# Performance work log

Hardware: AMD Instinct MI355X
Metric: run time of the kernel (lower is better)

The kernel has to match this reference:

```python
import jax, jax.numpy as jnp
import numpy as np


def _cdist_p2(x, y):
    # x: [B, N, D], y: [B, M, D] -> [B, N, M] euclidean distances
    x2 = jnp.sum(x * x, axis=-1, keepdims=True)          # [B, N, 1]
    y2 = jnp.sum(y * y, axis=-1, keepdims=True)          # [B, M, 1]
    xy = jnp.einsum('bnd,bmd->bnm', x, y)                # [B, N, M]
    d2 = x2 + jnp.swapaxes(y2, -1, -2) - 2.0 * xy
    return jnp.sqrt(jnp.maximum(d2, 0.0))


def setup_inputs() -> dict:
    key = jax.random.key(0)
    kx, ky = jax.random.split(key)
    B, N, M, D = 8, 8192, 8192, 64
    x = jax.random.normal(kx, (B, N, D), dtype=jnp.float32)
    y = jax.random.normal(ky, (B, M, D), dtype=jnp.float32)
    return {"x": x, "y": y}


def reference(x, y):
    # relative_distances: [B, N, M]
    rd = _cdist_p2(x, y)
    M = rd.shape[-1]
    a = jnp.min(rd, axis=-1)            # [B, N] nearest y for each x
    b = jnp.min(rd, axis=-2)            # [B, M] nearest x for each y
    loss_per_batch = jnp.sum(a, axis=-1) + jnp.sum(b, axis=-1)  # [B]
    return jnp.mean(loss_per_batch) / M
```

## Files before the change

### kernel.cpp

```cpp
#include <hip/hip_runtime.h>
#include <cstdint>
#include <cstddef>

typedef unsigned short u16;
typedef __attribute__((ext_vector_type(8))) short short8;
typedef __attribute__((ext_vector_type(8))) u16 ushort8;
typedef __attribute__((ext_vector_type(4))) float float4_t;

#define BB 8
#define NN 8192
#define DD 64
#define NTILES 64
#define TILE_SHORTS 8192

__device__ inline u16 f32_to_bf16(float f) {
  unsigned u = __float_as_uint(f);
  u += 0x7FFFu + ((u >> 16) & 1u);
  return (u16)(u >> 16);
}

__device__ inline unsigned enc_ord(float f) {
  unsigned u = __float_as_uint(f);
  return (u & 0x80000000u) ? ~u : (u | 0x80000000u);
}
__device__ inline float dec_ord(unsigned u) {
  return __uint_as_float((u & 0x80000000u) ? (u & 0x7fffffffu) : ~u);
}

__global__ __launch_bounds__(256) void pre_kernel(
    const float* __restrict__ x, const float* __restrict__ y,
    u16* __restrict__ xs, u16* __restrict__ ys,
    float* __restrict__ x2h, float* __restrict__ y2h,
    unsigned* __restrict__ colmax_u, const int use_part)
{
  const int bid = blockIdx.x;
  const int tid = threadIdx.x;

  if (!use_part && bid < 256) colmax_u[(bid << 8) | tid] = 0u;

  const bool isY = bid >= 1024;
  const float* src = isY ? y : x;
  u16* dst = isY ? ys : xs;
  float* s2 = isY ? y2h : x2h;

  const int row = ((bid & 1023) << 6) | (tid >> 2);
  const int kq  = tid & 3;

  const float4* rp = (const float4*)(src + (size_t)row * DD + kq * 16);
  float buf[16];
  float ss = 0.f;
#pragma unroll
  for (int k = 0; k < 4; ++k) {
    float4 f = rp[k];
    buf[4*k+0] = f.x; buf[4*k+1] = f.y; buf[4*k+2] = f.z; buf[4*k+3] = f.w;
    ss += f.x*f.x + f.y*f.y + f.z*f.z + f.w*f.w;
  }
  ss += __shfl_xor(ss, 1);
  ss += __shfl_xor(ss, 2);
  if (kq == 0) s2[row] = 0.5f * ss;

  const int b  = row >> 13;
  const int n  = row & (NN - 1);
  const int nt = n >> 7;
  const int I  = (n >> 4) & 7;
  const int rl = n & 15;
  const int s  = kq >> 1;
  const int qq0 = (kq & 1) * 2;
  u16* tb = dst + (size_t)((b << 6) | nt) * TILE_SHORTS;
#pragma unroll
  for (int t = 0; t < 2; ++t) {
    ushort8 o;
#pragma unroll
    for (int j = 0; j < 8; ++j) o[j] = f32_to_bf16(buf[t*8 + j]);
    *(ushort8*)(tb + (I*2 + s)*512 + ((qq0 + t)*16 + rl)*8) = o;
  }
}

__global__ __launch_bounds__(256, 2) void main_kernel(
    const u16* __restrict__ xs, const u16* __restrict__ ys,
    const float* __restrict__ x2h, const float* __restrict__ y2h,
    float* __restrict__ a_min, float* __restrict__ colpart,
    unsigned* __restrict__ colmax_u, const int use_part)
{
  __shared__ float rowbuf[4][128];

  const int bid = blockIdx.x;
  const int b   = bid & 7;
  const int nt  = bid >> 3;
  const int tid = threadIdx.x;
  const int w = tid >> 6, lane = tid & 63;
  const int l15 = lane & 15, q = lane >> 4;
  const int n0 = nt << 7;

  const u16* xs_tile = xs + (size_t)((b << 6) | nt) * TILE_SHORTS;
  short8 afr[8][2];
#pragma unroll
  for (int i = 0; i < 8; ++i)
#pragma unroll
    for (int s = 0; s < 2; ++s)
      afr[i][s] = *(const short8*)(xs_tile + (i*2 + s)*512 + lane*8);

  float4_t negx2[8];
  const float* x2b = x2h + b*NN + n0;
#pragma unroll
  for (int i = 0; i < 8; ++i) {
    float4_t v = *(const float4_t*)(x2b + i*16 + q*4);
    negx2[i] = {-v[0], -v[1], -v[2], -v[3]};
  }

  float rowmax[8][4];
#pragma unroll
  for (int i = 0; i < 8; ++i)
#pragma unroll
    for (int r = 0; r < 4; ++r) rowmax[i][r] = -3.0e38f;

  const float* y2b = y2h + b*NN;
  const u16* ys_b  = ys + (size_t)(b << 6) * TILE_SHORTS;
  float* colp      = colpart + (size_t)((b << 6) | nt) * NN;
  unsigned* colu   = colmax_u + b*NN;

  short8 bcur[2][2];
  float y2cur[2];
#pragma unroll
  for (int j = 0; j < 2; ++j) {
#pragma unroll
    for (int s = 0; s < 2; ++s)
      bcur[j][s] = *(const short8*)(ys_b + ((2*w + j)*2 + s)*512 + lane*8);
    y2cur[j] = y2b[w*32 + j*16 + l15];
  }

  for (int mt = 0; mt < NTILES; ++mt) {
    const int mtn = (mt + 1 < NTILES) ? (mt + 1) : 0;
    short8 bnext[2][2];
    float y2next[2];
    const u16* g = ys_b + (size_t)mtn * TILE_SHORTS;
#pragma unroll
    for (int j = 0; j < 2; ++j) {
#pragma unroll
      for (int s = 0; s < 2; ++s)
        bnext[j][s] = *(const short8*)(g + ((2*w + j)*2 + s)*512 + lane*8);
      y2next[j] = y2b[mtn*128 + w*32 + j*16 + l15];
    }

    float cmax[2];
#pragma unroll
    for (int j = 0; j < 2; ++j) {
      float4_t acc[8];
#pragma unroll
      for (int i = 0; i < 8; ++i)
        acc[i] = __builtin_amdgcn_mfma_f32_16x16x32_bf16(afr[i][0], bcur[j][0], negx2[i], 0, 0, 0);
#pragma unroll
      for (int i = 0; i < 8; ++i)
        acc[i] = __builtin_amdgcn_mfma_f32_16x16x32_bf16(afr[i][1], bcur[j][1], acc[i], 0, 0, 0);

      float m01 = fmaxf(fmaxf(acc[0][0], acc[0][1]), fmaxf(acc[0][2], acc[0][3]));
#pragma unroll
      for (int i = 1; i < 8; ++i) {
        float mi = fmaxf(fmaxf(acc[i][0], acc[i][1]), fmaxf(acc[i][2], acc[i][3]));
        m01 = fmaxf(m01, mi);
      }
      cmax[j] = m01;

      const float y2j = y2cur[j];
#pragma unroll
      for (int i = 0; i < 8; ++i)
#pragma unroll
        for (int r = 0; r < 4; ++r)
          rowmax[i][r] = fmaxf(rowmax[i][r], acc[i][r] - y2j);
    }

#pragma unroll
    for (int j = 0; j < 2; ++j) {
      cmax[j] = fmaxf(cmax[j], __shfl_xor(cmax[j], 16));
      cmax[j] = fmaxf(cmax[j], __shfl_xor(cmax[j], 32));
    }
    float cv = (q & 1) ? cmax[1] : cmax[0];
    const int m = (mt << 7) + w*32 + q*16 + l15;
    if (q < 2) {
      if (use_part) colp[m] = cv;
      else          atomicMax(&colu[m], enc_ord(cv));
    }

#pragma unroll
    for (int j = 0; j < 2; ++j) {
#pragma unroll
      for (int s = 0; s < 2; ++s) bcur[j][s] = bnext[j][s];
      y2cur[j] = y2next[j];
    }
  }

#pragma unroll
  for (int i = 0; i < 8; ++i)
#pragma unroll
    for (int r = 0; r < 4; ++r) {
      float v = rowmax[i][r];
      v = fmaxf(v, __shfl_xor(v, 1));
      v = fmaxf(v, __shfl_xor(v, 2));
      v = fmaxf(v, __shfl_xor(v, 4));
      v = fmaxf(v, __shfl_xor(v, 8));
      rowmax[i][r] = v;
    }
  if (l15 == 0) {
#pragma unroll
    for (int i = 0; i < 8; ++i)
#pragma unroll
      for (int r = 0; r < 4; ++r)
        rowbuf[w][i*16 + q*4 + r] = rowmax[i][r];
  }
  __syncthreads();
  if (tid < 128) {
    float v = fmaxf(fmaxf(rowbuf[0][tid], rowbuf[1][tid]),
                    fmaxf(rowbuf[2][tid], rowbuf[3][tid]));
    a_min[b*NN + n0 + tid] = sqrtf(fmaxf(-2.f * v, 0.f));
  }
}

__global__ __launch_bounds__(256) void reduce_kernel(
    const float* __restrict__ colpart, const unsigned* __restrict__ colmax_u,
    const float* __restrict__ y2h, const float* __restrict__ a_min,
    float* __restrict__ partials, const int use_part)
{
  const int bid = blockIdx.x;
  const int tid = threadIdx.x;
  const int g = bid*256 + tid;
  const int b = g >> 13, m = g & (NN - 1);

  float vc;
  if (use_part) {
    vc = -3.0e38f;
#pragma unroll 8
    for (int nt = 0; nt < 64; ++nt)
      vc = fmaxf(vc, colpart[(size_t)((b << 6) | nt) * NN + m]);
  } else {
    vc = dec_ord(colmax_u[g]);
  }
  float s = sqrtf(fmaxf(2.f*(y2h[g] - vc), 0.f))
          + a_min[g];

#pragma unroll
  for (int d = 1; d < 64; d <<= 1) s += __shfl_xor(s, d);
  __shared__ float wsum[4];
  if ((tid & 63) == 0) wsum[tid >> 6] = s;
  __syncthreads();
  if (tid == 0) partials[bid] = wsum[0] + wsum[1] + wsum[2] + wsum[3];
}

__global__ void final_kernel(const float* __restrict__ partials, float* __restrict__ out) {
  const int tid = threadIdx.x;
  float s = partials[tid];
#pragma unroll
  for (int d = 1; d < 64; d <<= 1) s += __shfl_xor(s, d);
  __shared__ float wsum[4];
  if ((tid & 63) == 0) wsum[tid >> 6] = s;
  __syncthreads();
  if (tid == 0) out[0] = (wsum[0] + wsum[1] + wsum[2] + wsum[3]) * (1.0f / 65536.0f);
}

extern "C" void kernel_launch(void* const* d_in, const int* in_sizes, int n_in,
                              void* d_out, int out_size, void* d_ws, size_t ws_size,
                              hipStream_t stream) {
  const float* x = (const float*)d_in[0];
  const float* y = (const float*)d_in[1];
  float* out = (float*)d_out;

  char* p = (char*)d_ws;
  u16* xs = (u16*)p;            p += (size_t)512 * 16384;
  u16* ys = (u16*)p;            p += (size_t)512 * 16384;
  float* x2h = (float*)p;       p += (size_t)65536 * 4;
  float* y2h = (float*)p;       p += (size_t)65536 * 4;
  float* a_min = (float*)p;     p += (size_t)65536 * 4;
  float* partials = (float*)p;  p += 4096;
  char* tail = p;
  float* colpart = (float*)tail;
  unsigned* colmax_u = (unsigned*)tail;
  const size_t need_part = (size_t)(tail - (char*)d_ws) + (size_t)512 * 8192 * 4;
  const int use_part = (ws_size >= need_part) ? 1 : 0;

  pre_kernel<<<dim3(2048), dim3(256), 0, stream>>>(x, y, xs, ys, x2h, y2h,
                                                   colmax_u, use_part);
  main_kernel<<<dim3(512), dim3(256), 0, stream>>>(xs, ys, x2h, y2h, a_min,
                                                   colpart, colmax_u, use_part);
  reduce_kernel<<<dim3(256), dim3(256), 0, stream>>>(colpart, colmax_u, y2h,
                                                     a_min, partials, use_part);
  final_kernel<<<dim3(1), dim3(256), 0, stream>>>(partials, out);
}
```

Before: 168.8 us.

## Software-pipeline MFMA with epilogue, use atomic column max, drop final kernel

The main loop is restructured so the MFMA stage for one 16-column half overlaps the max-reduction epilogue of the other half, using two accumulator sets. The column-max path always uses atomicMax on order-encoded uints instead of writing a large per-tile partial buffer that the reduce kernel re-scans. The final kernel is removed and the reduce kernel atomically adds into the output, which pre_kernel zeroes. pre_kernel also gains coalesced loads laid out to match the tile layout. Costs: more registers for the doubled accumulators, atomic contention on column maxima, and a nondeterministic float summation order.

```diff
diff --git a/kernel.cpp b/kernel.cpp
--- a/kernel.cpp
+++ b/kernel.cpp
@@ -31,56 +31,63 @@
     const float* __restrict__ x, const float* __restrict__ y,
     u16* __restrict__ xs, u16* __restrict__ ys,
     float* __restrict__ x2h, float* __restrict__ y2h,
-    unsigned* __restrict__ colmax_u, const int use_part)
+    unsigned* __restrict__ colmax_u, float* __restrict__ out)
 {
   const int bid = blockIdx.x;
   const int tid = threadIdx.x;
 
-  if (!use_part && bid < 256) colmax_u[(bid << 8) | tid] = 0u;
+  if (bid < 256) colmax_u[(bid << 8) | tid] = 0u;
+  if (bid == 0 && tid == 0) out[0] = 0.f;
 
   const bool isY = bid >= 1024;
   const float* src = isY ? y : x;
   u16* dst = isY ? ys : xs;
   float* s2 = isY ? y2h : x2h;
 
-  const int row = ((bid & 1023) << 6) | (tid >> 2);
-  const int kq  = tid & 3;
-
-  const float4* rp = (const float4*)(src + (size_t)row * DD + kq * 16);
-  float buf[16];
-  float ss = 0.f;
-#pragma unroll
-  for (int k = 0; k < 4; ++k) {
-    float4 f = rp[k];
-    buf[4*k+0] = f.x; buf[4*k+1] = f.y; buf[4*k+2] = f.z; buf[4*k+3] = f.w;
-    ss += f.x*f.x + f.y*f.y + f.z*f.z + f.w*f.w;
-  }
-  ss += __shfl_xor(ss, 1);
-  ss += __shfl_xor(ss, 2);
-  if (kq == 0) s2[row] = 0.5f * ss;
-
-  const int b  = row >> 13;
-  const int n  = row & (NN - 1);
-  const int nt = n >> 7;
-  const int I  = (n >> 4) & 7;
-  const int rl = n & 15;
-  const int s  = kq >> 1;
-  const int qq0 = (kq & 1) * 2;
-  u16* tb = dst + (size_t)((b << 6) | nt) * TILE_SHORTS;
-#pragma unroll
-  for (int t = 0; t < 2; ++t) {
-    ushort8 o;
-#pragma unroll
-    for (int j = 0; j < 8; ++j) o[j] = f32_to_bf16(buf[t*8 + j]);
-    *(ushort8*)(tb + (I*2 + s)*512 + ((qq0 + t)*16 + rl)*8) = o;
+  const int base = (bid & 1023) << 6;
+
+  {
+    const int w = tid >> 6, lane = tid & 63;
+    const int qq = lane >> 4, rl = lane & 15;
+    const int grow = base + w*16 + rl;
+    const int b  = grow >> 13;
+    const int n  = grow & (NN - 1);
+    const int nt = n >> 7;
+    const int I  = (n >> 4) & 7;
+    u16* tb = dst + (size_t)((b << 6) | nt) * TILE_SHORTS;
+#pragma unroll
+    for (int s = 0; s < 2; ++s) {
+      const float4* rp = (const float4*)(src + (size_t)grow * DD + s*32 + qq*8);
+      float4 f0 = rp[0], f1 = rp[1];
+      ushort8 o;
+      o[0] = f32_to_bf16(f0.x); o[1] = f32_to_bf16(f0.y);
+      o[2] = f32_to_bf16(f0.z); o[3] = f32_to_bf16(f0.w);
+      o[4] = f32_to_bf16(f1.x); o[5] = f32_to_bf16(f1.y);
+      o[6] = f32_to_bf16(f1.z); o[7] = f32_to_bf16(f1.w);
+      *(ushort8*)(tb + (I*2 + s)*512 + lane*8) = o;
+    }
+  }
+
+  {
+    const int row = base | (tid >> 2);
+    const int kq  = tid & 3;
+    const float4* rp = (const float4*)(src + (size_t)row * DD + kq * 16);
+    float ss = 0.f;
+#pragma unroll
+    for (int k = 0; k < 4; ++k) {
+      float4 f = rp[k];
+      ss += f.x*f.x + f.y*f.y + f.z*f.z + f.w*f.w;
+    }
+    ss += __shfl_xor(ss, 1);
+    ss += __shfl_xor(ss, 2);
+    if (kq == 0) s2[row] = 0.5f * ss;
   }
 }
 
 __global__ __launch_bounds__(256, 2) void main_kernel(
     const u16* __restrict__ xs, const u16* __restrict__ ys,
     const float* __restrict__ x2h, const float* __restrict__ y2h,
-    float* __restrict__ a_min, float* __restrict__ colpart,
-    unsigned* __restrict__ colmax_u, const int use_part)
+    float* __restrict__ a_min, unsigned* __restrict__ colmax_u)
 {
   __shared__ float rowbuf[4][128];
 
@@ -116,78 +123,73 @@
 
   const float* y2b = y2h + b*NN;
   const u16* ys_b  = ys + (size_t)(b << 6) * TILE_SHORTS;
-  float* colp      = colpart + (size_t)((b << 6) | nt) * NN;
   unsigned* colu   = colmax_u + b*NN;
 
-  short8 bcur[2][2];
-  float y2cur[2];
-#pragma unroll
-  for (int j = 0; j < 2; ++j) {
-#pragma unroll
-    for (int s = 0; s < 2; ++s)
-      bcur[j][s] = *(const short8*)(ys_b + ((2*w + j)*2 + s)*512 + lane*8);
-    y2cur[j] = y2b[w*32 + j*16 + l15];
-  }
-
-  for (int mt = 0; mt < NTILES; ++mt) {
-    const int mtn = (mt + 1 < NTILES) ? (mt + 1) : 0;
-    short8 bnext[2][2];
-    float y2next[2];
-    const u16* g = ys_b + (size_t)mtn * TILE_SHORTS;
-#pragma unroll
-    for (int j = 0; j < 2; ++j) {
-#pragma unroll
-      for (int s = 0; s < 2; ++s)
-        bnext[j][s] = *(const short8*)(g + ((2*w + j)*2 + s)*512 + lane*8);
-      y2next[j] = y2b[mtn*128 + w*32 + j*16 + l15];
-    }
-
-    float cmax[2];
-#pragma unroll
-    for (int j = 0; j < 2; ++j) {
-      float4_t acc[8];
-#pragma unroll
-      for (int i = 0; i < 8; ++i)
-        acc[i] = __builtin_amdgcn_mfma_f32_16x16x32_bf16(afr[i][0], bcur[j][0], negx2[i], 0, 0, 0);
-#pragma unroll
-      for (int i = 0; i < 8; ++i)
-        acc[i] = __builtin_amdgcn_mfma_f32_16x16x32_bf16(afr[i][1], bcur[j][1], acc[i], 0, 0, 0);
-
-      float m01 = fmaxf(fmaxf(acc[0][0], acc[0][1]), fmaxf(acc[0][2], acc[0][3]));
-#pragma unroll
-      for (int i = 1; i < 8; ++i) {
-        float mi = fmaxf(fmaxf(acc[i][0], acc[i][1]), fmaxf(acc[i][2], acc[i][3]));
-        m01 = fmaxf(m01, mi);
-      }
-      cmax[j] = m01;
-
-      const float y2j = y2cur[j];
-#pragma unroll
-      for (int i = 0; i < 8; ++i)
-#pragma unroll
-        for (int r = 0; r < 4; ++r)
-          rowmax[i][r] = fmaxf(rowmax[i][r], acc[i][r] - y2j);
-    }
-
-#pragma unroll
-    for (int j = 0; j < 2; ++j) {
-      cmax[j] = fmaxf(cmax[j], __shfl_xor(cmax[j], 16));
-      cmax[j] = fmaxf(cmax[j], __shfl_xor(cmax[j], 32));
-    }
-    float cv = (q & 1) ? cmax[1] : cmax[0];
-    const int m = (mt << 7) + w*32 + q*16 + l15;
-    if (q < 2) {
-      if (use_part) colp[m] = cv;
-      else          atomicMax(&colu[m], enc_ord(cv));
-    }
-
-#pragma unroll
-    for (int j = 0; j < 2; ++j) {
-#pragma unroll
-      for (int s = 0; s < 2; ++s) bcur[j][s] = bnext[j][s];
-      y2cur[j] = y2next[j];
-    }
-  }
+#define MFMA_STAGE(ACC, B0, B1)                                                \
+  do {                                                                         \
+    _Pragma("unroll") for (int i = 0; i < 8; ++i)                              \
+      ACC[i] = __builtin_amdgcn_mfma_f32_16x16x32_bf16(afr[i][0], B0, negx2[i], 0, 0, 0); \
+    _Pragma("unroll") for (int i = 0; i < 8; ++i)                              \
+      ACC[i] = __builtin_amdgcn_mfma_f32_16x16x32_bf16(afr[i][1], B1, ACC[i], 0, 0, 0);   \
+  } while (0)
+
+#define EPI(ACC, Y2V, MBASE)                                                   \
+  do {                                                                         \
+    float cm = fmaxf(fmaxf(ACC[0][0], ACC[0][1]), fmaxf(ACC[0][2], ACC[0][3]));\
+    _Pragma("unroll") for (int i = 1; i < 8; ++i) {                            \
+      float mi = fmaxf(fmaxf(ACC[i][0], ACC[i][1]), fmaxf(ACC[i][2], ACC[i][3]));\
+      cm = fmaxf(cm, mi);                                                      \
+    }                                                                          \
+    cm = fmaxf(cm, __shfl_xor(cm, 16));                                        \
+    cm = fmaxf(cm, __shfl_xor(cm, 32));                                        \
+    if (q == 0) atomicMax(&colu[(MBASE) + l15], enc_ord(cm));                  \
+    _Pragma("unroll") for (int i = 0; i < 8; ++i)                              \
+      _Pragma("unroll") for (int r = 0; r < 4; ++r)                            \
+        rowmax[i][r] = fmaxf(rowmax[i][r], ACC[i][r] - (Y2V));                 \
+  } while (0)
+
+  short8 bcur0[2], bcur1[2], bnx0[2], bnx1[2];
+  float y2c0, y2c1;
+  {
+    const u16* g = ys_b;
+    bcur0[0] = *(const short8*)(g + ((2*w + 0)*2 + 0)*512 + lane*8);
+    bcur0[1] = *(const short8*)(g + ((2*w + 0)*2 + 1)*512 + lane*8);
+    bcur1[0] = *(const short8*)(g + ((2*w + 1)*2 + 0)*512 + lane*8);
+    bcur1[1] = *(const short8*)(g + ((2*w + 1)*2 + 1)*512 + lane*8);
+    y2c0 = y2b[w*32 + l15];
+    y2c1 = y2b[w*32 + 16 + l15];
+  }
+  float4_t accA[8], accB[8];
+  MFMA_STAGE(accA, bcur0[0], bcur0[1]);
+  float y2A = y2c0;
+
+  for (int mt = 0; mt < NTILES - 1; ++mt) {
+    const u16* g = ys_b + (size_t)(mt + 1) * TILE_SHORTS;
+    bnx0[0] = *(const short8*)(g + ((2*w + 0)*2 + 0)*512 + lane*8);
+    bnx0[1] = *(const short8*)(g + ((2*w + 0)*2 + 1)*512 + lane*8);
+    bnx1[0] = *(const short8*)(g + ((2*w + 1)*2 + 0)*512 + lane*8);
+    bnx1[1] = *(const short8*)(g + ((2*w + 1)*2 + 1)*512 + lane*8);
+    float y2n0 = y2b[(mt + 1)*128 + w*32 + l15];
+    float y2n1 = y2b[(mt + 1)*128 + w*32 + 16 + l15];
+
+    MFMA_STAGE(accB, bcur1[0], bcur1[1]);
+    EPI(accA, y2A, (mt << 7) + w*32);
+
+    bcur0[0] = bnx0[0]; bcur0[1] = bnx0[1];
+    bcur1[0] = bnx1[0]; bcur1[1] = bnx1[1];
+    const float y2Bv = y2c1;
+    y2c0 = y2n0; y2c1 = y2n1;
+
+    MFMA_STAGE(accA, bcur0[0], bcur0[1]);
+    y2A = y2c0;
+    EPI(accB, y2Bv, (mt << 7) + w*32 + 16);
+  }
+  MFMA_STAGE(accB, bcur1[0], bcur1[1]);
+  EPI(accA, y2A, ((NTILES - 1) << 7) + w*32);
+  EPI(accB, y2c1, ((NTILES - 1) << 7) + w*32 + 16);
+
+#undef MFMA_STAGE
+#undef EPI
 
 #pragma unroll
   for (int i = 0; i < 8; ++i)
@@ -216,24 +218,14 @@
 }
 
 __global__ __launch_bounds__(256) void reduce_kernel(
-    const float* __restrict__ colpart, const unsigned* __restrict__ colmax_u,
-    const float* __restrict__ y2h, const float* __restrict__ a_min,
-    float* __restrict__ partials, const int use_part)
+    const unsigned* __restrict__ colmax_u, const float* __restrict__ y2h,
+    const float* __restrict__ a_min, float* __restrict__ out)
 {
   const int bid = blockIdx.x;
   const int tid = threadIdx.x;
   const int g = bid*256 + tid;
-  const int b = g >> 13, m = g & (NN - 1);
-
-  float vc;
-  if (use_part) {
-    vc = -3.0e38f;
-#pragma unroll 8
-    for (int nt = 0; nt < 64; ++nt)
-      vc = fmaxf(vc, colpart[(size_t)((b << 6) | nt) * NN + m]);
-  } else {
-    vc = dec_ord(colmax_u[g]);
-  }
+
+  float vc = dec_ord(colmax_u[g]);
   float s = sqrtf(fmaxf(2.f*(y2h[g] - vc), 0.f))
           + a_min[g];
 
@@ -242,18 +234,8 @@
   __shared__ float wsum[4];
   if ((tid & 63) == 0) wsum[tid >> 6] = s;
   __syncthreads();
-  if (tid == 0) partials[bid] = wsum[0] + wsum[1] + wsum[2] + wsum[3];
-}
-
-__global__ void final_kernel(const float* __restrict__ partials, float* __restrict__ out) {
-  const int tid = threadIdx.x;
-  float s = partials[tid];
-#pragma unroll
-  for (int d = 1; d < 64; d <<= 1) s += __shfl_xor(s, d);
-  __shared__ float wsum[4];
-  if ((tid & 63) == 0) wsum[tid >> 6] = s;
-  __syncthreads();
-  if (tid == 0) out[0] = (wsum[0] + wsum[1] + wsum[2] + wsum[3]) * (1.0f / 65536.0f);
+  if (tid == 0)
+    atomicAdd(out, (wsum[0] + wsum[1] + wsum[2] + wsum[3]) * (1.0f / 65536.0f));
 }
 
 extern "C" void kernel_launch(void* const* d_in, const int* in_sizes, int n_in,
@@ -269,18 +251,11 @@
   float* x2h = (float*)p;       p += (size_t)65536 * 4;
   float* y2h = (float*)p;       p += (size_t)65536 * 4;
   float* a_min = (float*)p;     p += (size_t)65536 * 4;
-  float* partials = (float*)p;  p += 4096;
-  char* tail = p;
-  float* colpart = (float*)tail;
-  unsigned* colmax_u = (unsigned*)tail;
-  const size_t need_part = (size_t)(tail - (char*)d_ws) + (size_t)512 * 8192 * 4;
-  const int use_part = (ws_size >= need_part) ? 1 : 0;
+  unsigned* colmax_u = (unsigned*)p;
 
   pre_kernel<<<dim3(2048), dim3(256), 0, stream>>>(x, y, xs, ys, x2h, y2h,
-                                                   colmax_u, use_part);
+                                                   colmax_u, out);
   main_kernel<<<dim3(512), dim3(256), 0, stream>>>(xs, ys, x2h, y2h, a_min,
-                                                   colpart, colmax_u, use_part);
-  reduce_kernel<<<dim3(256), dim3(256), 0, stream>>>(colpart, colmax_u, y2h,
-                                                     a_min, partials, use_part);
-  final_kernel<<<dim3(1), dim3(256), 0, stream>>>(partials, out);
-}
+                                                   colmax_u);
+  reduce_kernel<<<dim3(256), dim3(256), 0, stream>>>(colmax_u, y2h, a_min, out);
+}
```

New measurement: 240.4 us. 1.42x slower.
